# Optimization experiments

Hardware: AMD Instinct MI355X
Metric: run time of the kernel (lower is better)

The kernel has to match this reference:

```python
import jax, jax.numpy as jnp
import numpy as np


def _banded_diag_mean(a, b, r):
    """For each (batch i, row j) return mean of (a[i] @ b[i].T)[j, j-r:j+r+1],
    computed without materializing the LxL matrix. Windows are clipped to
    [max(0,j-r), min(L, j+r+1)].  a, b: [B, L, D]."""
    B, L, _ = a.shape
    sums = jnp.zeros((B, L), a.dtype)
    counts = jnp.zeros((L,), a.dtype)
    for d in range(-r, r + 1):  # small fixed set of 2r+1 diagonals
        if d >= 0:
            dots = jnp.einsum('bld,bld->bl', a[:, :L - d], b[:, d:])
            sums = sums.at[:, :L - d].add(dots)
            counts = counts.at[:L - d].add(1.0)
        else:
            dots = jnp.einsum('bld,bld->bl', a[:, -d:], b[:, :L + d])
            sums = sums.at[:, -d:].add(dots)
            counts = counts.at[-d:].add(1.0)
    return sums / counts


def setup_inputs() -> dict:
    key = jax.random.key(0)
    k1, k2, k3 = jax.random.split(key, 3)
    B, L, D_in, D_feat = 8, 1024, 512, 256
    return {
        'feature1': jax.random.normal(k1, (B, L, D_in), jnp.float32),
        'feature2': jax.random.normal(k2, (B, L, D_in), jnp.float32),
        'W': jax.random.normal(k3, (D_in, D_feat), jnp.float32) / np.sqrt(D_in),
        'b': jnp.zeros((D_feat,), jnp.float32),
        'positive_range_self': 4,
        'positive_range_tgt': 4,
    }


def reference(feature1, feature2, W, b, positive_range_self, positive_range_tgt):
    # MLPLayer projection (shared eval_func for both inputs): linear + relu
    emb_1 = jax.nn.relu(feature1 @ W + b)  # [B, L, Df]
    emb_2 = jax.nn.relu(feature2 @ W + b)  # [B, L, Df]
    B, L, Df = emb_1.shape
    N = B * L

    positive = jnp.einsum('bld,bld->bl', emb_1, emb_2)  # [B, L]
    if positive_range_self > 0:
        positive = positive + _banded_diag_mean(emb_1, emb_1, positive_range_self)
        positive = positive + _banded_diag_mean(emb_2, emb_2, positive_range_self)
    if positive_range_tgt > 0:
        positive = positive + _banded_diag_mean(emb_1, emb_2, positive_range_tgt)
    positive = positive.reshape(N)

    e1 = emb_1.reshape(N, Df)
    e2 = emb_2.reshape(N, Df)
    sim_matrix = e1 @ e2.T  # [N, N]
    negative = jax.nn.logsumexp(sim_matrix, axis=-1) - jnp.log(jnp.asarray(N, sim_matrix.dtype))

    nce_loss = jnp.mean(-positive + negative)
    return nce_loss
```

## Files before the change

kernel.cpp:

```cpp
#include <hip/hip_runtime.h>
#include <hip/hip_bf16.h>
#include <math.h>

#define DIN 512
#define DF 256
#define LSEQ 1024
#define NTOT 8192

typedef __attribute__((ext_vector_type(8))) short short8;
typedef __attribute__((ext_vector_type(4))) short short4v;
typedef __attribute__((ext_vector_type(4))) float f32x4;

__device__ __forceinline__ short f2bf(float x) {
  union { float f; unsigned u; } un; un.f = x;
  unsigned r = un.u + 0x7fffu + ((un.u >> 16) & 1u);
  return (short)(r >> 16);
}
__device__ __forceinline__ float bf2f(short s) {
  union { unsigned u; float f; } un; un.u = ((unsigned)(unsigned short)s) << 16;
  return un.f;
}

typedef __attribute__((address_space(1))) const unsigned char AS1c;
typedef __attribute__((address_space(3))) unsigned char AS3;
__device__ __forceinline__ void gload16(const void* g, void* l) {
  __builtin_amdgcn_global_load_lds((AS1c*)g, (AS3*)l, 16, 0, 0);
}
#define CFENCE() asm volatile("" ::: "memory")

__global__ __launch_bounds__(256) void prep_w_kernel(const float* __restrict__ W,
                                                     short* __restrict__ Wt) {
  int idx = blockIdx.x * 256 + threadIdx.x;
  int c = idx >> 9;
  int k = idx & (DIN - 1);
  Wt[idx] = f2bf(W[(size_t)k * DF + c]);
}

#define PBM 64
#define PBK 64
#define PROW 72

__global__ __launch_bounds__(256) void proj_kernel(const float* __restrict__ f1,
                                                   const float* __restrict__ f2,
                                                   const short* __restrict__ Wt,
                                                   const float* __restrict__ bias,
                                                   short* __restrict__ emb1,
                                                   short* __restrict__ emb2) {
  const float* feat = blockIdx.y ? f2 : f1;
  short* emb = blockIdx.y ? emb2 : emb1;
  __shared__ short ldsA[PBM * PROW];
  __shared__ short ldsB[DF * PROW];
  const int tid = threadIdx.x;
  const int lane = tid & 63, wv = tid >> 6;
  const int wrow = (wv & 1) * 32, wcol = (wv >> 1) * 128;
  const int l15 = lane & 15, lk = (lane >> 4) * 8;
  const int rowbase = blockIdx.x * PBM;

  f32x4 acc[2][8];
#pragma unroll
  for (int mi = 0; mi < 2; ++mi)
#pragma unroll
    for (int nf = 0; nf < 8; ++nf) acc[mi][nf] = f32x4{0.f, 0.f, 0.f, 0.f};

  for (int kb = 0; kb < DIN; kb += PBK) {
    __syncthreads();
#pragma unroll
    for (int i = 0; i < 4; ++i) {
      int flat = tid * 4 + i;
      int r = flat >> 4, kq = (flat & 15) * 4;
      f32x4 v = *(const f32x4*)(feat + (size_t)(rowbase + r) * DIN + kb + kq);
      short4v h;
      h[0] = f2bf(v[0]); h[1] = f2bf(v[1]); h[2] = f2bf(v[2]); h[3] = f2bf(v[3]);
      *(short4v*)(ldsA + r * PROW + kq) = h;
    }
#pragma unroll
    for (int i = 0; i < 8; ++i) {
      int c = tid, kq = i * 8;
      short8 v = *(const short8*)(Wt + (size_t)c * DIN + kb + kq);
      *(short8*)(ldsB + c * PROW + kq) = v;
    }
    __syncthreads();
#pragma unroll
    for (int kk = 0; kk < 2; ++kk) {
      short8 af[2], bf[8];
#pragma unroll
      for (int mi = 0; mi < 2; ++mi)
        af[mi] = *(const short8*)(ldsA + (wrow + mi * 16 + l15) * PROW + kk * 32 + lk);
#pragma unroll
      for (int nf = 0; nf < 8; ++nf)
        bf[nf] = *(const short8*)(ldsB + (wcol + nf * 16 + l15) * PROW + kk * 32 + lk);
#pragma unroll
      for (int mi = 0; mi < 2; ++mi)
#pragma unroll
        for (int nf = 0; nf < 8; ++nf)
          acc[mi][nf] = __builtin_amdgcn_mfma_f32_16x16x32_bf16(af[mi], bf[nf], acc[mi][nf], 0, 0, 0);
    }
  }
  const int r4 = (lane >> 4) * 4;
#pragma unroll
  for (int mi = 0; mi < 2; ++mi) {
    int row0 = rowbase + wrow + mi * 16 + r4;
#pragma unroll
    for (int nf = 0; nf < 8; ++nf) {
      int col = wcol + nf * 16 + l15;
      float bb = bias[col];
#pragma unroll
      for (int r = 0; r < 4; ++r) {
        float v = acc[mi][nf][r] + bb;
        v = v > 0.f ? v : 0.f;
        emb[(size_t)(row0 + r) * DF + col] = f2bf(v);
      }
    }
  }
}

__global__ __launch_bounds__(64) void positive_kernel(const short* __restrict__ emb1,
                                                      const short* __restrict__ emb2,
                                                      const int* __restrict__ prs,
                                                      const int* __restrict__ prt,
                                                      float* __restrict__ pos) {
  const int row = blockIdx.x;
  const int b = row >> 10, j = row & (LSEQ - 1);
  const int lane = threadIdx.x;
  const int rs = prs[0], rt = prt[0];
  float a1[4], a2[4];
  {
    short4v v1 = *(const short4v*)(emb1 + (size_t)row * DF + lane * 4);
    short4v v2 = *(const short4v*)(emb2 + (size_t)row * DF + lane * 4);
#pragma unroll
    for (int i = 0; i < 4; ++i) { a1[i] = bf2f(v1[i]); a2[i] = bf2f(v2[i]); }
  }
  float dot12 = 0.f, p11 = 0.f, p22 = 0.f, p12 = 0.f;
#pragma unroll
  for (int i = 0; i < 4; ++i) dot12 += a1[i] * a2[i];
  int rmax = rs > rt ? rs : rt;
  for (int d = -rmax; d <= rmax; ++d) {
    int k = j + d;
    if (k < 0 || k >= LSEQ) continue;
    size_t koff = (size_t)(b * LSEQ + k) * DF + lane * 4;
    short4v w1 = *(const short4v*)(emb1 + koff);
    short4v w2 = *(const short4v*)(emb2 + koff);
    float d11 = 0.f, d22 = 0.f, d12 = 0.f;
#pragma unroll
    for (int i = 0; i < 4; ++i) {
      float e1k = bf2f(w1[i]), e2k = bf2f(w2[i]);
      d11 += a1[i] * e1k;
      d22 += a2[i] * e2k;
      d12 += a1[i] * e2k;
    }
    if (d >= -rs && d <= rs) { p11 += d11; p22 += d22; }
    if (d >= -rt && d <= rt) { p12 += d12; }
  }
#pragma unroll
  for (int m = 1; m < 64; m <<= 1) {
    dot12 += __shfl_xor(dot12, m);
    p11 += __shfl_xor(p11, m);
    p22 += __shfl_xor(p22, m);
    p12 += __shfl_xor(p12, m);
  }
  if (lane == 0) {
    float res = dot12;
    if (rs > 0) {
      int lo = j - rs < 0 ? 0 : j - rs;
      int hi = j + rs > LSEQ - 1 ? LSEQ - 1 : j + rs;
      res += (p11 + p22) / (float)(hi - lo + 1);
    }
    if (rt > 0) {
      int lo = j - rt < 0 ? 0 : j - rt;
      int hi = j + rt > LSEQ - 1 ? LSEQ - 1 : j + rt;
      res += p12 / (float)(hi - lo + 1);
    }
    pos[row] = res;
  }
}

#define NBM 256
#define NBN 64
#define NCHUNK 16
#define CHW (NTOT / NCHUNK)
#define NT (CHW / NBN)

__global__ __launch_bounds__(256, 2) void negative_kernel(const short* __restrict__ e1,
                                                          const short* __restrict__ e2,
                                                          float* __restrict__ mpart,
                                                          float* __restrict__ spart) {
  __shared__ short ldsB[2][NBN * DF];
  const int tid = threadIdx.x;
  const int lane = tid & 63, wv = tid >> 6;
  const int l15 = lane & 15, lk16 = lane >> 4;
  const int rowbase = blockIdx.x * NBM + wv * 64;
  const short* colbase = e2 + (size_t)(blockIdx.y * CHW) * DF;

  auto stage = [&](int tt) {
    const short* nb = colbase + (size_t)tt * NBN * DF;
    short* db = (short*)ldsB[tt & 1];
#pragma unroll
    for (int i = 0; i < 8; ++i) {
      int L = i * 256 + tid;
      int c = L >> 5, s = L & 31;
      int kb = s ^ (c & 31);
      gload16(nb + (size_t)c * DF + kb * 8, db + (i * 256 + wv * 64) * 8);
    }
  };

  stage(0);
  CFENCE();
  short8 a[4][8];
#pragma unroll
  for (int mi = 0; mi < 4; ++mi)
#pragma unroll
    for (int ks = 0; ks < 8; ++ks)
      a[mi][ks] = *(const short8*)(e1 + (size_t)(rowbase + mi * 16 + l15) * DF + ks * 32 + lk16 * 8);
  CFENCE();
  stage(1);
  CFENCE();

  float mrun[16], srun[16];
#pragma unroll
  for (int i = 0; i < 16; ++i) { mrun[i] = -1e30f; srun[i] = 0.f; }

  for (int t = 0; t < NT; ++t) {
    if (t < NT - 1) asm volatile("s_waitcnt vmcnt(8)" ::: "memory");
    else            asm volatile("s_waitcnt vmcnt(0)" ::: "memory");
    __builtin_amdgcn_sched_barrier(0);
    __builtin_amdgcn_s_barrier();
    const short* buf = (const short*)ldsB[t & 1];

    f32x4 acc[4][4];
#pragma unroll
    for (int mi = 0; mi < 4; ++mi)
#pragma unroll
      for (int nf = 0; nf < 4; ++nf) acc[mi][nf] = f32x4{0.f, 0.f, 0.f, 0.f};

#pragma unroll
    for (int nfp = 0; nfp < 2; ++nfp) {
      __builtin_amdgcn_s_setprio(1);
#pragma unroll
      for (int ks = 0; ks < 8; ++ks) {
        int kblk = ks * 4 + lk16;
        int c0 = (2 * nfp) * 16 + l15;
        int c1 = (2 * nfp + 1) * 16 + l15;
        short8 b0 = *(const short8*)(buf + (c0 * 32 + (kblk ^ (c0 & 31))) * 8);
        short8 b1 = *(const short8*)(buf + (c1 * 32 + (kblk ^ (c1 & 31))) * 8);
#pragma unroll
        for (int mi = 0; mi < 4; ++mi) {
          acc[mi][2 * nfp] = __builtin_amdgcn_mfma_f32_16x16x32_bf16(a[mi][ks], b0, acc[mi][2 * nfp], 0, 0, 0);
          acc[mi][2 * nfp + 1] = __builtin_amdgcn_mfma_f32_16x16x32_bf16(a[mi][ks], b1, acc[mi][2 * nfp + 1], 0, 0, 0);
        }
      }
      __builtin_amdgcn_s_setprio(0);
#pragma unroll
      for (int mi = 0; mi < 4; ++mi)
#pragma unroll
        for (int r = 0; r < 4; ++r) {
          int s8 = mi * 4 + r;
          float v0 = acc[mi][2 * nfp][r], v1 = acc[mi][2 * nfp + 1][r];
          float mx = fmaxf(v0, v1);
          float mo = mrun[s8];
          if (mx > mo + 8.f) {
            srun[s8] *= __expf(mo - mx);
            mo = mx;
            mrun[s8] = mx;
          }
          srun[s8] += __expf(v0 - mo) + __expf(v1 - mo);
        }
    }
    __builtin_amdgcn_s_barrier();
    CFENCE();
    if (t + 2 < NT) stage(t + 2);
  }

#pragma unroll
  for (int mi = 0; mi < 4; ++mi)
#pragma unroll
    for (int r = 0; r < 4; ++r) {
      int s8 = mi * 4 + r;
      float m = mrun[s8], s = srun[s8];
#pragma unroll
      for (int msk = 1; msk < 16; msk <<= 1) {
        float mo = __shfl_xor(m, msk);
        float so = __shfl_xor(s, msk);
        float mn = fmaxf(m, mo);
        s = s * __expf(m - mn) + so * __expf(mo - mn);
        m = mn;
      }
      if (l15 == 0) {
        int row = rowbase + mi * 16 + lk16 * 4 + r;
        mpart[blockIdx.y * NTOT + row] = m;
        spart[blockIdx.y * NTOT + row] = s;
      }
    }
}

__global__ __launch_bounds__(256) void finalize1_kernel(const float* __restrict__ pos,
                                                        const float* __restrict__ mpart,
                                                        const float* __restrict__ spart,
                                                        float* __restrict__ partial) {
  __shared__ float red[4];
  int row = blockIdx.x * 256 + threadIdx.x;
  float m = -1e30f;
#pragma unroll
  for (int c = 0; c < NCHUNK; ++c) m = fmaxf(m, mpart[c * NTOT + row]);
  float s = 0.f;
#pragma unroll
  for (int c = 0; c < NCHUNK; ++c) s += spart[c * NTOT + row] * __expf(mpart[c * NTOT + row] - m);
  float v = m + logf(s) - pos[row];
#pragma unroll
  for (int msk = 1; msk < 64; msk <<= 1) v += __shfl_xor(v, msk);
  if ((threadIdx.x & 63) == 0) red[threadIdx.x >> 6] = v;
  __syncthreads();
  if (threadIdx.x == 0) partial[blockIdx.x] = red[0] + red[1] + red[2] + red[3];
}

__global__ __launch_bounds__(64) void finalize2_kernel(const float* __restrict__ partial,
                                                       float* __restrict__ out) {
  int lane = threadIdx.x;
  float v = lane < 32 ? partial[lane] : 0.f;
#pragma unroll
  for (int msk = 1; msk < 64; msk <<= 1) v += __shfl_xor(v, msk);
  if (lane == 0) out[0] = v / (float)NTOT - logf((float)NTOT);
}

extern "C" void kernel_launch(void* const* d_in, const int* in_sizes, int n_in,
                              void* d_out, int out_size, void* d_ws, size_t ws_size,
                              hipStream_t stream) {
  const float* f1 = (const float*)d_in[0];
  const float* f2 = (const float*)d_in[1];
  const float* W = (const float*)d_in[2];
  const float* bias = (const float*)d_in[3];
  const int* prs = (const int*)d_in[4];
  const int* prt = (const int*)d_in[5];
  float* out = (float*)d_out;

  char* ws = (char*)d_ws;
  short* Wt = (short*)(ws);
  short* emb1 = (short*)(ws + 262144);
  short* emb2 = (short*)(ws + 262144 + 4194304);
  float* pos = (float*)(ws + 8650752);
  float* mpart = (float*)(ws + 8683520);
  float* spart = (float*)(ws + 9207808);
  float* partial = (float*)(ws + 9732096);

  prep_w_kernel<<<(DF * DIN) / 256, 256, 0, stream>>>(W, Wt);
  proj_kernel<<<dim3(NTOT / PBM, 2), 256, 0, stream>>>(f1, f2, Wt, bias, emb1, emb2);
  positive_kernel<<<NTOT, 64, 0, stream>>>(emb1, emb2, prs, prt, pos);
  negative_kernel<<<dim3(NTOT / NBM, NCHUNK), 256, 0, stream>>>(emb1, emb2, mpart, spart);
  finalize1_kernel<<<32, 256, 0, stream>>>(pos, mpart, spart, partial);
  finalize2_kernel<<<1, 64, 0, stream>>>(partial, out);
}
```

Measured before the change: 107.1 us.

## Shrink negative-kernel tiles, reorganize LDS layout, and simplify online logsumexp

Halves the row and column tile sizes of the sim-matrix logsumexp kernel (each wave now covers 32 rows and 32 columns per step) and raises occupancy to 3 blocks per SIMD. The LDS staging layout drops the XOR swizzle in favour of a k-major layout with simpler addressing. The online max/sum update becomes branchless, rescaling every step. Smaller tiles mean less register use and more parallelism, but lower MFMA reuse per B load, twice as many loop iterations and barriers, and an extra exp per element per step.

```diff
diff --git a/kernel.cpp b/kernel.cpp
--- a/kernel.cpp
+++ b/kernel.cpp
@@ -174,13 +174,13 @@
   }
 }
 
-#define NBM 256
-#define NBN 64
+#define NBM 128
+#define NBN 32
 #define NCHUNK 16
 #define CHW (NTOT / NCHUNK)
 #define NT (CHW / NBN)
 
-__global__ __launch_bounds__(256, 2) void negative_kernel(const short* __restrict__ e1,
+__global__ __launch_bounds__(256, 3) void negative_kernel(const short* __restrict__ e1,
                                                           const short* __restrict__ e2,
                                                           float* __restrict__ mpart,
                                                           float* __restrict__ spart) {
@@ -188,26 +188,25 @@
   const int tid = threadIdx.x;
   const int lane = tid & 63, wv = tid >> 6;
   const int l15 = lane & 15, lk16 = lane >> 4;
-  const int rowbase = blockIdx.x * NBM + wv * 64;
+  const int rowbase = blockIdx.x * NBM + wv * 32;
   const short* colbase = e2 + (size_t)(blockIdx.y * CHW) * DF;
 
+  const int src_off = (tid & 31) * DF + (tid >> 5) * 8;
+  const int dst_off = wv * 512;
+
   auto stage = [&](int tt) {
-    const short* nb = colbase + (size_t)tt * NBN * DF;
-    short* db = (short*)ldsB[tt & 1];
-#pragma unroll
-    for (int i = 0; i < 8; ++i) {
-      int L = i * 256 + tid;
-      int c = L >> 5, s = L & 31;
-      int kb = s ^ (c & 31);
-      gload16(nb + (size_t)c * DF + kb * 8, db + (i * 256 + wv * 64) * 8);
-    }
+    const short* nb = colbase + (size_t)tt * NBN * DF + src_off;
+    short* db = (short*)ldsB[tt & 1] + dst_off;
+#pragma unroll
+    for (int i = 0; i < 4; ++i)
+      gload16(nb + i * 64, db + i * 2048);
   };
 
   stage(0);
   CFENCE();
-  short8 a[4][8];
-#pragma unroll
-  for (int mi = 0; mi < 4; ++mi)
+  short8 a[2][8];
+#pragma unroll
+  for (int mi = 0; mi < 2; ++mi)
 #pragma unroll
     for (int ks = 0; ks < 8; ++ks)
       a[mi][ks] = *(const short8*)(e1 + (size_t)(rowbase + mi * 16 + l15) * DF + ks * 32 + lk16 * 8);
@@ -215,63 +214,53 @@
   stage(1);
   CFENCE();
 
-  float mrun[16], srun[16];
-#pragma unroll
-  for (int i = 0; i < 16; ++i) { mrun[i] = -1e30f; srun[i] = 0.f; }
+  float mrun[8], srun[8];
+#pragma unroll
+  for (int i = 0; i < 8; ++i) { mrun[i] = -1e30f; srun[i] = 0.f; }
 
   for (int t = 0; t < NT; ++t) {
-    if (t < NT - 1) asm volatile("s_waitcnt vmcnt(8)" ::: "memory");
+    if (t < NT - 1) asm volatile("s_waitcnt vmcnt(4)" ::: "memory");
     else            asm volatile("s_waitcnt vmcnt(0)" ::: "memory");
-    __builtin_amdgcn_sched_barrier(0);
     __builtin_amdgcn_s_barrier();
-    const short* buf = (const short*)ldsB[t & 1];
-
-    f32x4 acc[4][4];
-#pragma unroll
-    for (int mi = 0; mi < 4; ++mi)
-#pragma unroll
-      for (int nf = 0; nf < 4; ++nf) acc[mi][nf] = f32x4{0.f, 0.f, 0.f, 0.f};
-
-#pragma unroll
-    for (int nfp = 0; nfp < 2; ++nfp) {
-      __builtin_amdgcn_s_setprio(1);
-#pragma unroll
-      for (int ks = 0; ks < 8; ++ks) {
-        int kblk = ks * 4 + lk16;
-        int c0 = (2 * nfp) * 16 + l15;
-        int c1 = (2 * nfp + 1) * 16 + l15;
-        short8 b0 = *(const short8*)(buf + (c0 * 32 + (kblk ^ (c0 & 31))) * 8);
-        short8 b1 = *(const short8*)(buf + (c1 * 32 + (kblk ^ (c1 & 31))) * 8);
-#pragma unroll
-        for (int mi = 0; mi < 4; ++mi) {
-          acc[mi][2 * nfp] = __builtin_amdgcn_mfma_f32_16x16x32_bf16(a[mi][ks], b0, acc[mi][2 * nfp], 0, 0, 0);
-          acc[mi][2 * nfp + 1] = __builtin_amdgcn_mfma_f32_16x16x32_bf16(a[mi][ks], b1, acc[mi][2 * nfp + 1], 0, 0, 0);
-        }
-      }
-      __builtin_amdgcn_s_setprio(0);
-#pragma unroll
-      for (int mi = 0; mi < 4; ++mi)
-#pragma unroll
-        for (int r = 0; r < 4; ++r) {
-          int s8 = mi * 4 + r;
-          float v0 = acc[mi][2 * nfp][r], v1 = acc[mi][2 * nfp + 1][r];
-          float mx = fmaxf(v0, v1);
-          float mo = mrun[s8];
-          if (mx > mo + 8.f) {
-            srun[s8] *= __expf(mo - mx);
-            mo = mx;
-            mrun[s8] = mx;
-          }
-          srun[s8] += __expf(v0 - mo) + __expf(v1 - mo);
-        }
-    }
+    const short* bbase = (const short*)ldsB[t & 1] + lk16 * 256 + l15 * 8;
+
+    f32x4 acc[2][2];
+#pragma unroll
+    for (int mi = 0; mi < 2; ++mi)
+#pragma unroll
+      for (int nf = 0; nf < 2; ++nf) acc[mi][nf] = f32x4{0.f, 0.f, 0.f, 0.f};
+
+    __builtin_amdgcn_s_setprio(1);
+#pragma unroll
+    for (int ks = 0; ks < 8; ++ks) {
+      short8 b0 = *(const short8*)(bbase + ks * 1024);
+      short8 b1 = *(const short8*)(bbase + ks * 1024 + 128);
+#pragma unroll
+      for (int mi = 0; mi < 2; ++mi) {
+        acc[mi][0] = __builtin_amdgcn_mfma_f32_16x16x32_bf16(a[mi][ks], b0, acc[mi][0], 0, 0, 0);
+        acc[mi][1] = __builtin_amdgcn_mfma_f32_16x16x32_bf16(a[mi][ks], b1, acc[mi][1], 0, 0, 0);
+      }
+    }
+    __builtin_amdgcn_s_setprio(0);
+
+#pragma unroll
+    for (int mi = 0; mi < 2; ++mi)
+#pragma unroll
+      for (int r = 0; r < 4; ++r) {
+        int s8 = mi * 4 + r;
+        float v0 = acc[mi][0][r], v1 = acc[mi][1][r];
+        float mo = mrun[s8];
+        float mn = fmaxf(mo, fmaxf(v0, v1));
+        mrun[s8] = mn;
+        srun[s8] = srun[s8] * __expf(mo - mn) + __expf(v0 - mn) + __expf(v1 - mn);
+      }
     __builtin_amdgcn_s_barrier();
     CFENCE();
     if (t + 2 < NT) stage(t + 2);
   }
 
 #pragma unroll
-  for (int mi = 0; mi < 4; ++mi)
+  for (int mi = 0; mi < 2; ++mi)
 #pragma unroll
     for (int r = 0; r < 4; ++r) {
       int s8 = mi * 4 + r;
```

Result: faster. 93.96 us (-12.2%).
